# Kernel tuning notes

Measured on AMD Instinct MI355X. Metric: run time of the kernel, lower is better.

The kernel has to match this reference:

```python
import jax, jax.numpy as jnp
import numpy as np

B, NU, NY, NX, NW, T = 32, 64, 64, 512, 512, 1024


def setup_inputs() -> dict:
    key = jax.random.key(0)
    ks = jax.random.split(key, 12)
    inp = {}
    inp["u"] = jax.random.normal(ks[0], (B, NU, T), dtype=jnp.float32)
    # parameters (E init = I per module; small random weights keep the 1024-step
    # nonlinear recurrence numerically stable)
    inp["E"] = jnp.eye(NX, dtype=jnp.float32) + 0.01 * jax.random.normal(ks[1], (NX, NX), dtype=jnp.float32)
    inp["F_w"] = jax.random.normal(ks[2], (NX, NX), dtype=jnp.float32) * (0.3 / np.sqrt(NX))
    inp["F_b"] = jnp.zeros((NX,), dtype=jnp.float32)
    inp["B1_w"] = jax.random.normal(ks[3], (NX, NW), dtype=jnp.float32) * (0.3 / np.sqrt(NW))
    inp["B2_w"] = jax.random.normal(ks[4], (NX, NU), dtype=jnp.float32) * (1.0 / np.sqrt(NU))
    inp["C2tild"] = jax.random.normal(ks[5], (NW, NX), dtype=jnp.float32) / np.sqrt(NX)
    inp["bv"] = jax.random.uniform(ks[6], (NW,), dtype=jnp.float32) - 0.5
    inp["Dtild"] = jax.random.normal(ks[7], (NW, NU), dtype=jnp.float32) / np.sqrt(NU)
    inp["C1_w"] = jax.random.normal(ks[8], (NY, NX), dtype=jnp.float32) * (1.0 / np.sqrt(NX))
    inp["D11_w"] = jax.random.normal(ks[9], (NY, NW), dtype=jnp.float32) * (1.0 / np.sqrt(NW))
    inp["D12_w"] = jax.random.normal(ks[10], (NY, NU), dtype=jnp.float32) * (1.0 / np.sqrt(NU))
    inp["by"] = jnp.zeros((NY,), dtype=jnp.float32)
    inp["multis"] = jnp.ones((NW,), dtype=jnp.float32)  # IQC_multipliers (Neuron)
    return inp


def reference(u, E, F_w, F_b, B1_w, B2_w, C2tild, bv, Dtild, C1_w, D11_w, D12_w, by, multis):
    inputs = jnp.transpose(u, (0, 2, 1))            # (b, T, nu)
    b = inputs.shape[0]
    nx = E.shape[0]
    Einv = jnp.linalg.inv(E)
    Cv = C2tild / multis[:, None]                    # diag(1/multis) @ C2tild
    Dv = Dtild / multis[:, None]
    h0 = jnp.zeros((b, nx), dtype=u.dtype)

    def step(ht, ut):
        vt = ht @ Cv.T + ut @ Dv.T + bv              # (b, nw)
        wt = jax.nn.relu(vt)
        eh = ht @ F_w.T + F_b + wt @ B1_w.T + ut @ B2_w.T
        ht1 = eh @ Einv.T
        return ht1, ht1

    u_seq = jnp.swapaxes(inputs[:, :-1, :], 0, 1)    # (T-1, b, nu)
    _, hs = jax.lax.scan(step, h0, u_seq)            # (T-1, b, nx)
    states = jnp.swapaxes(jnp.concatenate([h0[None], hs], axis=0), 0, 1)  # (b, T, nx)

    W = jax.nn.relu(states @ Cv.T + inputs @ Dv.T + bv)   # (b, T, nw)
    yest = states @ C1_w.T + W @ D11_w.T + inputs @ D12_w.T + by  # (b, T, ny)
    return jnp.transpose(yest, (0, 2, 1))            # (b, ny, T)
```

## Files before the change

### kernel.cpp

```cpp
#include <hip/hip_runtime.h>

typedef _Float16 f16;
typedef _Float16 h2_t __attribute__((ext_vector_type(2)));
typedef _Float16 h8_t __attribute__((ext_vector_type(8)));
typedef float    f4_t __attribute__((ext_vector_type(4)));

__device__ __forceinline__ float fdot2u(unsigned int a, unsigned int b, float c) {
  return __builtin_amdgcn_fdot2(__builtin_bit_cast(h2_t, a),
                                __builtin_bit_cast(h2_t, b), c, false);
}

template<int F16OUT, int ACCUM, int RELU, int BIASF>
__global__ __launch_bounds__(256) void gemm16(
    const f16* __restrict__ Ap, long lda, long sAz,
    const f16* __restrict__ Bp, long ldb,
    void* __restrict__ Cp, long ldc, long sCz,
    const float* __restrict__ biasN,
    int M, int N, int K)
{
  const int lane = threadIdx.x & 63;
  const int wv   = threadIdx.x >> 6;
  const int rl = lane & 15, kb = lane >> 4;
  const long z = blockIdx.z;
  const f16* Az = Ap + z * sAz;
  const int rowA = blockIdx.x * 64 + wv * 16 + rl;
  const long rA = (rowA < M) ? rowA : 0;
  const int colBase = blockIdx.y * 64;
  f4_t acc[4];
  #pragma unroll
  for (int c = 0; c < 4; ++c) acc[c] = 0.0f;

  for (int k0 = 0; k0 < K; k0 += 32) {
    h8_t af = *(const h8_t*)(Az + rA * lda + (k0 + kb * 8));
    h8_t bf[4];
    #pragma unroll
    for (int i = 0; i < 8; ++i) {
      long krow = (long)(k0 + kb * 8 + i) * ldb + colBase + rl;
      #pragma unroll
      for (int c = 0; c < 4; ++c) bf[c][i] = Bp[krow + 16 * c];
    }
    #pragma unroll
    for (int c = 0; c < 4; ++c)
      acc[c] = __builtin_amdgcn_mfma_f32_16x16x32_f16(af, bf[c], acc[c], 0, 0, 0);
  }

  #pragma unroll
  for (int c = 0; c < 4; ++c) {
    const int col = colBase + c * 16 + rl;
    #pragma unroll
    for (int g = 0; g < 4; ++g) {
      const int row = blockIdx.x * 64 + wv * 16 + kb * 4 + g;
      if (row < M) {
        float v = acc[c][g];
        const long ci = z * sCz + (long)row * ldc + col;
        if (BIASF) v += biasN[col];
        if (ACCUM) v += F16OUT ? (float)((const f16*)Cp)[ci] : ((const float*)Cp)[ci];
        if (RELU) v = fmaxf(v, 0.0f);
        if (F16OUT) ((f16*)Cp)[ci] = (f16)v;
        else        ((float*)Cp)[ci] = v;
      }
    }
  }
}

__global__ void k_cvt(const float* __restrict__ s, f16* __restrict__ d, int n) {
  int i = blockIdx.x * 256 + threadIdx.x;
  if (i < n) d[i] = (f16)s[i];
}

__global__ void k_build_cv(const float* __restrict__ C2, const float* __restrict__ mul,
                           f16* __restrict__ cv) {
  int i = blockIdx.x * 256 + threadIdx.x;
  int r = i >> 9;
  cv[i] = (f16)(C2[i] / mul[r]);
}

__global__ void k_build_dvt(const float* __restrict__ Dt, const float* __restrict__ mul,
                            f16* __restrict__ dvt) {
  int i = blockIdx.x * 256 + threadIdx.x;
  int k = i >> 9, n = i & 511;
  dvt[i] = (f16)(Dt[n * 64 + k] / mul[n]);
}

__global__ void k_2im(const float* __restrict__ s, f16* __restrict__ d) {
  int i = blockIdx.x * 256 + threadIdx.x;
  int r = i >> 9, c = i & 511;
  d[i] = (f16)(((r == c) ? 2.0f : 0.0f) - s[i]);
}

__global__ void k_tr16(const f16* __restrict__ s, f16* __restrict__ d, int R, int C) {
  int i = blockIdx.x * 256 + threadIdx.x;
  if (i < R * C) { int j = i / R, r = i % R; d[i] = s[r * C + j]; }
}

__global__ void k_woutt(const float* __restrict__ C1, const float* __restrict__ D11,
                        const float* __restrict__ D12, f16* __restrict__ Wo) {
  int i = blockIdx.x * 256 + threadIdx.x;
  int k = i >> 6, j = i & 63;
  float v = (k < 512) ? C1[j * 512 + k]
          : (k < 1024) ? D11[j * 512 + (k - 512)]
                       : D12[j * 64 + (k - 1024)];
  Wo[i] = (f16)v;
}

__global__ void k_cb(const f16* __restrict__ X, const float* __restrict__ Fb,
                     float* __restrict__ cb) {
  int i = threadIdx.x;
  float a = 0.0f;
  for (int k = 0; k < 512; ++k) a += (float)X[i * 512 + k] * Fb[k];
  cb[i] = a;
}

__global__ void k_bias0(const f16* __restrict__ Cv, const float* __restrict__ cb,
                        const float* __restrict__ bv, float* __restrict__ b0) {
  int i = blockIdx.x * 512 + threadIdx.x;
  if (i < 512) b0[i] = cb[i];
  else {
    int j = i - 512;
    float a = bv[j];
    for (int k = 0; k < 512; ++k) a += (float)Cv[j * 512 + k] * cb[k];
    b0[i] = a;
  }
}

__global__ void k_packu(const float* __restrict__ u, f16* __restrict__ up) {
  __shared__ f16 tile[64][65];
  int b = blockIdx.y, t0 = blockIdx.x << 6;
  int tid = threadIdx.x;
  #pragma unroll
  for (int it = 0; it < 16; ++it) {
    int idx = it * 256 + tid; int i = idx >> 6, tt = idx & 63;
    tile[tt][i] = (f16)u[((long)b * 64 + i) * 1024 + t0 + tt];
  }
  __syncthreads();
  #pragma unroll
  for (int it = 0; it < 16; ++it) {
    int idx = it * 256 + tid; int tt = idx >> 6, i = idx & 63;
    up[((long)(t0 + tt) * 32 + b) * 64 + i] = tile[tt][i];
  }
}

__global__ void k_packw(const f16* __restrict__ A1, const f16* __restrict__ A2,
                        const f16* __restrict__ M1, const f16* __restrict__ M2,
                        unsigned int* __restrict__ Wp) {
  int U = blockIdx.x * 256 + threadIdx.x;
  int p = U & 3; int V = U >> 2;
  int tid = V & 511; int sj = V >> 9;
  int jj = sj & 31; int s = sj >> 5;
  int q = tid & 3, r = tid >> 2;
  int R = s * 128 + r;
  int k = q * 256 + jj * 8 + p * 2;
  f16 g0, g1;
  if (R < 512) {
    if (k < 512) { g0 = A1[R * 512 + k];         g1 = A1[R * 512 + k + 1]; }
    else         { g0 = A2[R * 512 + k - 512];   g1 = A2[R * 512 + k - 511]; }
  } else {
    int Rm = R - 512;
    if (k < 512) { g0 = M1[Rm * 512 + k];        g1 = M1[Rm * 512 + k + 1]; }
    else         { g0 = M2[Rm * 512 + k - 512];  g1 = M2[Rm * 512 + k - 511]; }
  }
  unsigned int lo = __builtin_bit_cast(unsigned short, g0);
  unsigned int hi = __builtin_bit_cast(unsigned short, g1);
  Wp[U] = lo | (hi << 16);
}

__global__ __launch_bounds__(512, 1) void k_scan(
    const uint4* __restrict__ Wp4,
    const f16* __restrict__ bHV,
    const float* __restrict__ b0,
    f16* __restrict__ Sst,
    unsigned int* __restrict__ flg)
{
  const int wg = blockIdx.x;
  const int s = wg >> 5, b = wg & 31;
  const int tid = threadIdx.x;
  const int q = tid & 3, r = tid >> 2;
  const int R = (s << 7) + r;
  const int lane = tid & 63;
  __shared__ __align__(16) unsigned int lds[4 * 132];

  uint4 wreg[32];
  #pragma unroll
  for (int j = 0; j < 32; ++j) wreg[j] = Wp4[(long)(s * 32 + j) * 512 + tid];
  #pragma unroll
  for (int j = 0; j < 32; ++j)
    asm volatile("" : "+v"(wreg[j].x), "+v"(wreg[j].y), "+v"(wreg[j].z), "+v"(wreg[j].w));

  const float b0r = b0[R];
  const bool isV = (s >= 4);
  unsigned int* SstU = (unsigned int*)Sst;
  const unsigned int* lp = lds + q * 132;

  for (int t = 1; t < 1024; ++t) {
    float bsv = (float)bHV[((long)(t - 1) * 32 + b) * 1024 + R];

    if (t > 1) {
      const unsigned int* fp = flg + ((long)(t - 1) * 32 + b) * 32;
      for (;;) {
        unsigned int v = 1u;
        if (lane < 8)
          v = __hip_atomic_load(fp + lane, __ATOMIC_RELAXED, __HIP_MEMORY_SCOPE_AGENT);
        if (__all(v != 0u)) break;
        __builtin_amdgcn_s_sleep(1);
      }
      asm volatile("" ::: "memory");
    }
    unsigned int sv = __hip_atomic_load(&SstU[((long)(t - 1) * 32 + b) * 512 + tid],
                                        __ATOMIC_RELAXED, __HIP_MEMORY_SCOPE_AGENT);
    lds[(tid >> 7) * 132 + (tid & 127)] = sv;
    __syncthreads();

    float acc = 0.0f;
    #pragma unroll
    for (int jj = 0; jj < 32; ++jj) {
      uint4 s4 = *(const uint4*)(lp + jj * 4);
      acc = fdot2u(s4.x, wreg[jj].x, acc);
      acc = fdot2u(s4.y, wreg[jj].y, acc);
      acc = fdot2u(s4.z, wreg[jj].z, acc);
      acc = fdot2u(s4.w, wreg[jj].w, acc);
    }
    acc += __shfl_xor(acc, 1, 64);
    acc += __shfl_xor(acc, 2, 64);

    float val = acc + bsv + b0r;
    if (isV) val = fmaxf(val, 0.0f);
    f16 hv = (f16)val;
    unsigned int hb = (unsigned int)__builtin_bit_cast(unsigned short, hv);
    unsigned int nb = __shfl_down(hb, 4, 64);
    if ((tid & 7) == 0) {
      __hip_atomic_store(&SstU[((long)t * 32 + b) * 512 + (R >> 1)], hb | (nb << 16),
                         __ATOMIC_RELAXED, __HIP_MEMORY_SCOPE_AGENT);
    }
    __syncthreads();
    if (tid == 0)
      __hip_atomic_store(flg + ((long)t * 32 + b) * 32 + s, 1u,
                         __ATOMIC_RELAXED, __HIP_MEMORY_SCOPE_AGENT);
  }
}

__global__ void k_trout(const float* __restrict__ C, float* __restrict__ out) {
  __shared__ float tile[64][65];
  int b = blockIdx.y, t0 = blockIdx.x << 6;
  int tid = threadIdx.x;
  #pragma unroll
  for (int it = 0; it < 16; ++it) {
    int idx = it * 256 + tid; int tt = idx >> 6, j = idx & 63;
    tile[j][tt] = C[((long)b * 1024 + t0 + tt) * 64 + j];
  }
  __syncthreads();
  #pragma unroll
  for (int it = 0; it < 16; ++it) {
    int idx = it * 256 + tid; int j = idx >> 6, tt = idx & 63;
    out[((long)b * 64 + j) * 1024 + t0 + tt] = tile[j][tt];
  }
}

extern "C" void kernel_launch(void* const* d_in, const int* in_sizes, int n_in,
                              void* d_out, int out_size, void* d_ws, size_t ws_size,
                              hipStream_t stream) {
  (void)in_sizes; (void)n_in; (void)out_size; (void)ws_size;
  const float* u   = (const float*)d_in[0];
  const float* E   = (const float*)d_in[1];
  const float* Fw  = (const float*)d_in[2];
  const float* Fb  = (const float*)d_in[3];
  const float* B1w = (const float*)d_in[4];
  const float* B2w = (const float*)d_in[5];
  const float* C2t = (const float*)d_in[6];
  const float* bv  = (const float*)d_in[7];
  const float* Dt  = (const float*)d_in[8];
  const float* C1w = (const float*)d_in[9];
  const float* D11 = (const float*)d_in[10];
  const float* D12 = (const float*)d_in[11];
  const float* by  = (const float*)d_in[12];
  const float* mul = (const float*)d_in[13];
  float* out = (float*)d_out;

  char* w = (char*)d_ws;
  size_t off = 0;
  auto alloc = [&](size_t bytes) { size_t o = off; off += (bytes + 255) & ~(size_t)255; return o; };

  f16*  UP    = (f16*)(w + alloc(1025L * 32 * 64 * 2));
  f16*  E16   = (f16*)(w + alloc(262144L * 2));
  f16*  F16   = (f16*)(w + alloc(262144L * 2));
  f16*  B116  = (f16*)(w + alloc(262144L * 2));
  f16*  B216  = (f16*)(w + alloc(32768L * 2));
  f16*  CV16  = (f16*)(w + alloc(262144L * 2));
  f16*  DVT   = (f16*)(w + alloc(32768L * 2));
  f16*  XA    = (f16*)(w + alloc(262144L * 2));
  f16*  XB    = (f16*)(w + alloc(262144L * 2));
  f16*  Z16   = (f16*)(w + alloc(262144L * 2));
  float* Y32  = (float*)(w + alloc(262144L * 4));
  f16*  A1    = (f16*)(w + alloc(262144L * 2));
  f16*  A2    = (f16*)(w + alloc(262144L * 2));
  f16*  A3    = (f16*)(w + alloc(32768L * 2));
  f16*  M1    = (f16*)(w + alloc(262144L * 2));
  f16*  M2    = (f16*)(w + alloc(262144L * 2));
  f16*  CVA3  = (f16*)(w + alloc(32768L * 2));
  f16*  A3T   = (f16*)(w + alloc(32768L * 2));
  f16*  CVA3T = (f16*)(w + alloc(32768L * 2));
  unsigned int* WPK = (unsigned int*)(w + alloc(524288L * 4));
  f16*  WOUT  = (f16*)(w + alloc(69632L * 2));
  float* CB   = (float*)(w + alloc(512L * 4));
  float* B0   = (float*)(w + alloc(1024L * 4));
  f16*  BHV   = (f16*)(w + alloc(1024L * 32 * 1024 * 2));
  f16*  SST   = (f16*)(w + alloc(1024L * 32 * 1024 * 2));
  float* C32  = (float*)(w + alloc(2097152L * 4));
  unsigned int* FLG = (unsigned int*)C32;

  (void)hipMemsetAsync(UP, 0, 1025L * 32 * 64 * 2, stream);
  (void)hipMemsetAsync(FLG, 0, 1024L * 32 * 32 * 4, stream);
  (void)hipMemsetAsync(SST, 0, 32L * 1024 * 2, stream);

  k_packu<<<dim3(16, 32), 256, 0, stream>>>(u, UP);
  k_cvt<<<1024, 256, 0, stream>>>(E, E16, 262144);
  k_cvt<<<1024, 256, 0, stream>>>(Fw, F16, 262144);
  k_cvt<<<1024, 256, 0, stream>>>(B1w, B116, 262144);
  k_cvt<<<128, 256, 0, stream>>>(B2w, B216, 32768);
  k_build_cv<<<1024, 256, 0, stream>>>(C2t, mul, CV16);
  k_build_dvt<<<128, 256, 0, stream>>>(Dt, mul, DVT);

  k_2im<<<1024, 256, 0, stream>>>(E, XA);
  f16 *X = XA, *Xo = XB;
  for (int it = 0; it < 4; ++it) {
    gemm16<0,0,0,0><<<dim3(8,8,1), 256, 0, stream>>>(E16, 512, 0, X, 512, Y32, 512, 0, nullptr, 512, 512, 512);
    k_2im<<<1024, 256, 0, stream>>>(Y32, Z16);
    gemm16<1,0,0,0><<<dim3(8,8,1), 256, 0, stream>>>(X, 512, 0, Z16, 512, Xo, 512, 0, nullptr, 512, 512, 512);
    f16* tmp = X; X = Xo; Xo = tmp;
  }

  gemm16<1,0,0,0><<<dim3(8,8,1), 256, 0, stream>>>(X, 512, 0, F16, 512, A1, 512, 0, nullptr, 512, 512, 512);
  gemm16<1,0,0,0><<<dim3(8,8,1), 256, 0, stream>>>(X, 512, 0, B116, 512, A2, 512, 0, nullptr, 512, 512, 512);
  gemm16<1,0,0,0><<<dim3(8,1,1), 256, 0, stream>>>(X, 512, 0, B216, 64, A3, 64, 0, nullptr, 512, 64, 512);
  gemm16<1,0,0,0><<<dim3(8,8,1), 256, 0, stream>>>(CV16, 512, 0, A1, 512, M1, 512, 0, nullptr, 512, 512, 512);
  gemm16<1,0,0,0><<<dim3(8,8,1), 256, 0, stream>>>(CV16, 512, 0, A2, 512, M2, 512, 0, nullptr, 512, 512, 512);
  gemm16<1,0,0,0><<<dim3(8,1,1), 256, 0, stream>>>(CV16, 512, 0, A3, 64, CVA3, 64, 0, nullptr, 512, 64, 512);
  k_tr16<<<128, 256, 0, stream>>>(A3, A3T, 512, 64);
  k_tr16<<<128, 256, 0, stream>>>(CVA3, CVA3T, 512, 64);
  k_woutt<<<272, 256, 0, stream>>>(C1w, D11, D12, WOUT);
  k_cb<<<1, 512, 0, stream>>>(X, Fb, CB);
  k_bias0<<<2, 512, 0, stream>>>(CV16, CB, bv, B0);
  k_packw<<<2048, 256, 0, stream>>>(A1, A2, M1, M2, WPK);

  gemm16<1,0,0,0><<<dim3(512,8,1), 256, 0, stream>>>(UP, 64, 0, A3T, 512, BHV, 1024, 0, nullptr, 32768, 512, 64);
  gemm16<1,0,0,0><<<dim3(512,8,1), 256, 0, stream>>>(UP, 64, 0, CVA3T, 512, BHV + 512, 1024, 0, nullptr, 32768, 512, 64);
  gemm16<1,1,0,0><<<dim3(512,8,1), 256, 0, stream>>>(UP + 2048, 64, 0, DVT, 512, BHV + 512, 1024, 0, nullptr, 32768, 512, 64);
  gemm16<1,0,1,1><<<dim3(1,8,1), 256, 0, stream>>>(UP, 64, 0, DVT, 512, SST + 512, 1024, 0, bv, 32, 512, 64);

  k_scan<<<256, 512, 0, stream>>>((const uint4*)WPK, BHV, B0, SST, FLG);

  gemm16<0,0,0,0><<<dim3(16,1,32), 256, 0, stream>>>(SST, 32768, 1024, WOUT, 64, C32, 64, 65536, nullptr, 1024, 64, 1024);
  gemm16<0,1,0,1><<<dim3(16,1,32), 256, 0, stream>>>(UP, 2048, 64, WOUT + 65536, 64, C32, 64, 65536, by, 1024, 64, 64);
  k_trout<<<dim3(16, 32), 256, 0, stream>>>(C32, out);
}
```

Before: 2.154 ms.

## Replace scan flag sync with tagged ring buffer and fuse setup kernels

```diff
diff --git a/kernel.cpp b/kernel.cpp
--- a/kernel.cpp
+++ b/kernel.cpp
@@ -63,9 +63,15 @@
   }
 }
 
-__global__ void k_cvt(const float* __restrict__ s, f16* __restrict__ d, int n) {
-  int i = blockIdx.x * 256 + threadIdx.x;
-  if (i < n) d[i] = (f16)s[i];
+__global__ void k_cvt4(const float* __restrict__ a, f16* __restrict__ da,
+                       const float* __restrict__ b, f16* __restrict__ db,
+                       const float* __restrict__ c, f16* __restrict__ dc,
+                       const float* __restrict__ d, f16* __restrict__ dd) {
+  int i = blockIdx.x * 256 + threadIdx.x;
+  if (i < 262144) da[i] = (f16)a[i];
+  else if (i < 524288) db[i - 262144] = (f16)b[i - 262144];
+  else if (i < 786432) dc[i - 524288] = (f16)c[i - 524288];
+  else if (i < 819200) dd[i - 786432] = (f16)d[i - 786432];
 }
 
 __global__ void k_build_cv(const float* __restrict__ C2, const float* __restrict__ mul,
@@ -136,7 +142,7 @@
   #pragma unroll
   for (int it = 0; it < 16; ++it) {
     int idx = it * 256 + tid; int tt = idx >> 6, i = idx & 63;
-    up[((long)(t0 + tt) * 32 + b) * 64 + i] = tile[tt][i];
+    up[((long)b * 1025 + t0 + tt) * 64 + i] = tile[tt][i];
   }
 }
 
@@ -164,20 +170,26 @@
   Wp[U] = lo | (hi << 16);
 }
 
+__global__ void k_tag0(const f16* __restrict__ W0, unsigned int* __restrict__ ring) {
+  int i = blockIdx.x * 256 + threadIdx.x;
+  int b = i >> 9, j = i & 511;
+  unsigned int bits = (unsigned int)__builtin_bit_cast(unsigned short, W0[i]);
+  ring[(long)b * 1024 + 512 + j] = bits << 16;
+}
+
 __global__ __launch_bounds__(512, 1) void k_scan(
     const uint4* __restrict__ Wp4,
     const f16* __restrict__ bHV,
     const float* __restrict__ b0,
-    f16* __restrict__ Sst,
-    unsigned int* __restrict__ flg)
+    unsigned int* __restrict__ ring,
+    unsigned int* __restrict__ hist)
 {
   const int wg = blockIdx.x;
   const int s = wg >> 5, b = wg & 31;
   const int tid = threadIdx.x;
   const int q = tid & 3, r = tid >> 2;
   const int R = (s << 7) + r;
-  const int lane = tid & 63;
-  __shared__ __align__(16) unsigned int lds[4 * 132];
+  __shared__ __align__(16) unsigned int lds[2 * 528];
 
   uint4 wreg[32];
   #pragma unroll
@@ -188,28 +200,24 @@
 
   const float b0r = b0[R];
   const bool isV = (s >= 4);
-  unsigned int* SstU = (unsigned int*)Sst;
-  const unsigned int* lp = lds + q * 132;
 
   for (int t = 1; t < 1024; ++t) {
-    float bsv = (float)bHV[((long)(t - 1) * 32 + b) * 1024 + R];
-
-    if (t > 1) {
-      const unsigned int* fp = flg + ((long)(t - 1) * 32 + b) * 32;
-      for (;;) {
-        unsigned int v = 1u;
-        if (lane < 8)
-          v = __hip_atomic_load(fp + lane, __ATOMIC_RELAXED, __HIP_MEMORY_SCOPE_AGENT);
-        if (__all(v != 0u)) break;
-        __builtin_amdgcn_s_sleep(1);
-      }
-      asm volatile("" ::: "memory");
-    }
-    unsigned int sv = __hip_atomic_load(&SstU[((long)(t - 1) * 32 + b) * 512 + tid],
-                                        __ATOMIC_RELAXED, __HIP_MEMORY_SCOPE_AGENT);
-    lds[(tid >> 7) * 132 + (tid & 127)] = sv;
+    float bsv = (float)bHV[((long)b * 1025 + (t - 1)) * 1024 + R];
+
+    const unsigned int* rp = ring + (((t - 1) & 3) * 32 + b) * 1024 + tid * 2;
+    const unsigned int tg = (unsigned int)(t - 1);
+    unsigned int d0, d1;
+    for (;;) {
+      d0 = __hip_atomic_load(rp,     __ATOMIC_RELAXED, __HIP_MEMORY_SCOPE_AGENT);
+      d1 = __hip_atomic_load(rp + 1, __ATOMIC_RELAXED, __HIP_MEMORY_SCOPE_AGENT);
+      if ((((d0 ^ tg) | (d1 ^ tg)) & 0xFFFFu) == 0u) break;
+    }
+    asm volatile("" ::: "memory");
+    unsigned int pk = (d0 >> 16) | (d1 & 0xFFFF0000u);
+    lds[(t & 1) * 528 + (tid >> 7) * 132 + (tid & 127)] = pk;
     __syncthreads();
 
+    const unsigned int* lp = lds + (t & 1) * 528 + q * 132;
     float acc = 0.0f;
     #pragma unroll
     for (int jj = 0; jj < 32; ++jj) {
@@ -226,15 +234,20 @@
     if (isV) val = fmaxf(val, 0.0f);
     f16 hv = (f16)val;
     unsigned int hb = (unsigned int)__builtin_bit_cast(unsigned short, hv);
-    unsigned int nb = __shfl_down(hb, 4, 64);
-    if ((tid & 7) == 0) {
-      __hip_atomic_store(&SstU[((long)t * 32 + b) * 512 + (R >> 1)], hb | (nb << 16),
-                         __ATOMIC_RELAXED, __HIP_MEMORY_SCOPE_AGENT);
-    }
-    __syncthreads();
-    if (tid == 0)
-      __hip_atomic_store(flg + ((long)t * 32 + b) * 32 + s, 1u,
-                         __ATOMIC_RELAXED, __HIP_MEMORY_SCOPE_AGENT);
+
+    if (s == 0)
+      hist[((long)(t - 1) * 32 + b) * 512 + tid] = pk;
+
+    if (t == 1023) {
+      unsigned int nb = __shfl_down(hb, 4, 64);
+      if ((tid & 7) == 0)
+        hist[((long)1023 * 32 + b) * 512 + (R >> 1)] = hb | (nb << 16);
+    } else {
+      if (q == 0)
+        __hip_atomic_store(ring + ((t & 3) * 32 + b) * 1024 + R,
+                           (hb << 16) | (unsigned int)t,
+                           __ATOMIC_RELAXED, __HIP_MEMORY_SCOPE_AGENT);
+    }
   }
 }
 
@@ -279,13 +292,15 @@
   size_t off = 0;
   auto alloc = [&](size_t bytes) { size_t o = off; off += (bytes + 255) & ~(size_t)255; return o; };
 
-  f16*  UP    = (f16*)(w + alloc(1025L * 32 * 64 * 2));
+  f16*  UP2   = (f16*)(w + alloc(32L * 1025 * 64 * 2));
   f16*  E16   = (f16*)(w + alloc(262144L * 2));
   f16*  F16   = (f16*)(w + alloc(262144L * 2));
   f16*  B116  = (f16*)(w + alloc(262144L * 2));
   f16*  B216  = (f16*)(w + alloc(32768L * 2));
   f16*  CV16  = (f16*)(w + alloc(262144L * 2));
-  f16*  DVT   = (f16*)(w + alloc(32768L * 2));
+  f16*  CATB  = (f16*)(w + alloc(65536L * 2));
+  f16*  CVA3T = CATB;
+  f16*  DVT   = CATB + 32768;
   f16*  XA    = (f16*)(w + alloc(262144L * 2));
   f16*  XB    = (f16*)(w + alloc(262144L * 2));
   f16*  Z16   = (f16*)(w + alloc(262144L * 2));
@@ -297,31 +312,27 @@
   f16*  M2    = (f16*)(w + alloc(262144L * 2));
   f16*  CVA3  = (f16*)(w + alloc(32768L * 2));
   f16*  A3T   = (f16*)(w + alloc(32768L * 2));
-  f16*  CVA3T = (f16*)(w + alloc(32768L * 2));
   unsigned int* WPK = (unsigned int*)(w + alloc(524288L * 4));
   f16*  WOUT  = (f16*)(w + alloc(69632L * 2));
   float* CB   = (float*)(w + alloc(512L * 4));
   float* B0   = (float*)(w + alloc(1024L * 4));
-  f16*  BHV   = (f16*)(w + alloc(1024L * 32 * 1024 * 2));
-  f16*  SST   = (f16*)(w + alloc(1024L * 32 * 1024 * 2));
+  f16*  W0    = (f16*)(w + alloc(16384L * 2));
+  unsigned int* RING = (unsigned int*)(w + alloc(4L * 32 * 1024 * 4));
+  f16*  BHV   = (f16*)(w + alloc(32L * 1025 * 1024 * 2));
+  unsigned int* HIST = (unsigned int*)(w + alloc(1024L * 32 * 512 * 4));
   float* C32  = (float*)(w + alloc(2097152L * 4));
-  unsigned int* FLG = (unsigned int*)C32;
-
-  (void)hipMemsetAsync(UP, 0, 1025L * 32 * 64 * 2, stream);
-  (void)hipMemsetAsync(FLG, 0, 1024L * 32 * 32 * 4, stream);
-  (void)hipMemsetAsync(SST, 0, 32L * 1024 * 2, stream);
-
-  k_packu<<<dim3(16, 32), 256, 0, stream>>>(u, UP);
-  k_cvt<<<1024, 256, 0, stream>>>(E, E16, 262144);
-  k_cvt<<<1024, 256, 0, stream>>>(Fw, F16, 262144);
-  k_cvt<<<1024, 256, 0, stream>>>(B1w, B116, 262144);
-  k_cvt<<<128, 256, 0, stream>>>(B2w, B216, 32768);
+
+  (void)hipMemsetAsync(UP2, 0, 32L * 1025 * 64 * 2, stream);
+  (void)hipMemsetAsync(RING, 0, 32L * 1024 * 4, stream);
+
+  k_packu<<<dim3(16, 32), 256, 0, stream>>>(u, UP2);
+  k_cvt4<<<3200, 256, 0, stream>>>(E, E16, Fw, F16, B1w, B116, B2w, B216);
   k_build_cv<<<1024, 256, 0, stream>>>(C2t, mul, CV16);
   k_build_dvt<<<128, 256, 0, stream>>>(Dt, mul, DVT);
 
   k_2im<<<1024, 256, 0, stream>>>(E, XA);
   f16 *X = XA, *Xo = XB;
-  for (int it = 0; it < 4; ++it) {
+  for (int it = 0; it < 3; ++it) {
     gemm16<0,0,0,0><<<dim3(8,8,1), 256, 0, stream>>>(E16, 512, 0, X, 512, Y32, 512, 0, nullptr, 512, 512, 512);
     k_2im<<<1024, 256, 0, stream>>>(Y32, Z16);
     gemm16<1,0,0,0><<<dim3(8,8,1), 256, 0, stream>>>(X, 512, 0, Z16, 512, Xo, 512, 0, nullptr, 512, 512, 512);
@@ -341,14 +352,14 @@
   k_bias0<<<2, 512, 0, stream>>>(CV16, CB, bv, B0);
   k_packw<<<2048, 256, 0, stream>>>(A1, A2, M1, M2, WPK);
 
-  gemm16<1,0,0,0><<<dim3(512,8,1), 256, 0, stream>>>(UP, 64, 0, A3T, 512, BHV, 1024, 0, nullptr, 32768, 512, 64);
-  gemm16<1,0,0,0><<<dim3(512,8,1), 256, 0, stream>>>(UP, 64, 0, CVA3T, 512, BHV + 512, 1024, 0, nullptr, 32768, 512, 64);
-  gemm16<1,1,0,0><<<dim3(512,8,1), 256, 0, stream>>>(UP + 2048, 64, 0, DVT, 512, BHV + 512, 1024, 0, nullptr, 32768, 512, 64);
-  gemm16<1,0,1,1><<<dim3(1,8,1), 256, 0, stream>>>(UP, 64, 0, DVT, 512, SST + 512, 1024, 0, bv, 32, 512, 64);
-
-  k_scan<<<256, 512, 0, stream>>>((const uint4*)WPK, BHV, B0, SST, FLG);
-
-  gemm16<0,0,0,0><<<dim3(16,1,32), 256, 0, stream>>>(SST, 32768, 1024, WOUT, 64, C32, 64, 65536, nullptr, 1024, 64, 1024);
-  gemm16<0,1,0,1><<<dim3(16,1,32), 256, 0, stream>>>(UP, 2048, 64, WOUT + 65536, 64, C32, 64, 65536, by, 1024, 64, 64);
+  gemm16<1,0,0,0><<<dim3(513,8,1), 256, 0, stream>>>(UP2, 64, 0, A3T, 512, BHV, 1024, 0, nullptr, 32800, 512, 64);
+  gemm16<1,0,0,0><<<dim3(513,8,1), 256, 0, stream>>>(UP2, 64, 0, CVA3T, 512, BHV + 512, 1024, 0, nullptr, 32800, 512, 128);
+  gemm16<1,0,1,1><<<dim3(1,8,32), 256, 0, stream>>>(UP2, 64, 65600, DVT, 512, W0, 512, 512, bv, 1, 512, 64);
+  k_tag0<<<64, 256, 0, stream>>>(W0, RING);
+
+  k_scan<<<256, 512, 0, stream>>>((const uint4*)WPK, BHV, B0, RING, HIST);
+
+  gemm16<0,0,0,0><<<dim3(16,1,32), 256, 0, stream>>>((const f16*)HIST, 32768, 1024, WOUT, 64, C32, 64, 65536, nullptr, 1024, 64, 1024);
+  gemm16<0,1,0,1><<<dim3(16,1,32), 256, 0, stream>>>(UP2, 64, 65600, WOUT + 65536, 64, C32, 64, 65536, by, 1024, 64, 64);
   k_trout<<<dim3(16, 32), 256, 0, stream>>>(C32, out);
 }
```

New measurement: 2.734 ms. 1.27x slower.
